# Kernel optimization log

Hardware: AMD Instinct MI355X
Metric: run time of the kernel (lower is better)

## Reference

```python
import jax, jax.numpy as jnp
import numpy as np

H, HK, D, BLK, GH = 32, 8, 96, 64, 128   # q heads, kv heads, head_dim, gate block, gate hidden
HIDDEN = 3072
THR = 0.03
NEG = -1e30

def _rot_half(x):
    h = x.shape[-1] // 2
    return jnp.concatenate([-x[..., h:], x[..., :h]], axis=-1)

def setup_inputs() -> dict:
    key = jax.random.key(0)
    ks = jax.random.split(key, 6)
    B, S = 1, 2048
    hidden_states = jax.random.normal(ks[0], (B, S, HIDDEN), dtype=jnp.float32)
    # RoPE tables, theta = 10000
    inv_freq = 1.0 / (10000.0 ** (np.arange(0, D, 2, dtype=np.float32) / D))
    t = np.arange(S, dtype=np.float32)
    freqs = np.outer(t, inv_freq)                   # [S, D/2]
    emb = np.concatenate([freqs, freqs], axis=-1)   # [S, D]
    cos = jnp.asarray(np.cos(emb), dtype=jnp.float32)
    sin = jnp.asarray(np.sin(emb), dtype=jnp.float32)
    op = H * D + 2 * HK * D
    qkv_w = jax.random.normal(ks[1], (HIDDEN, op), dtype=jnp.float32) * 0.02
    o_w = jax.random.normal(ks[2], (H * D, HIDDEN), dtype=jnp.float32) * 0.02
    gate_wq = jax.random.normal(ks[3], (D, GH), dtype=jnp.float32) * 0.05
    gate_wk = jax.random.normal(ks[4], (2 * D, GH), dtype=jnp.float32) * 0.05
    return dict(hidden_states=hidden_states, cos=cos, sin=sin,
                qkv_w=qkv_w, o_w=o_w, gate_wq=gate_wq, gate_wk=gate_wk)

def reference(hidden_states, cos, sin, qkv_w, o_w, gate_wq, gate_wk):
    B, S, _ = hidden_states.shape
    G = H // HK            # GQA group size
    nB = S // BLK          # number of gate blocks
    scale = D ** -0.5

    # fused QKV projection and head split
    qkv = hidden_states @ qkv_w
    q = qkv[..., : H * D].reshape(B, S, H, D)
    k = qkv[..., H * D : H * D + HK * D].reshape(B, S, HK, D)
    v = qkv[..., H * D + HK * D :].reshape(B, S, HK, D)
    q_nope, k_nope = q, k

    # RoPE (unsqueeze over head dim)
    cs = cos[None, :, None, :]
    sn = sin[None, :, None, :]
    q = q * cs + _rot_half(q) * sn
    k = k * cs + _rot_half(k) * sn

    # ---- learned block-sparse gate (SeerAttention AttnGate) ----
    kb = k_nope.reshape(B, nB, BLK, HK, D)
    k_pool = jnp.concatenate([kb.mean(2), kb.max(2)], axis=-1)      # [B,nB,HK,2D] avg+max seq pooling
    k_gate = jnp.einsum('bnhe,eg->bnhg', k_pool, gate_wk)
    q_pool = q_nope.reshape(B, S, HK, G, D).mean(3)                 # q-head pooling to kv heads
    q_pool = q_pool.reshape(B, nB, BLK, HK, D).mean(2)              # block pooling
    q_gate = jnp.einsum('bnhd,dg->bnhg', q_pool, gate_wq)
    gate_logits = jnp.einsum('bqhg,bkhg->bhqk', q_gate, k_gate) * (GH ** -0.5)
    blk_causal = jnp.tril(jnp.ones((nB, nB), dtype=bool))
    gate_logits = jnp.where(blk_causal, gate_logits, NEG)
    gate_probs = jax.nn.softmax(gate_logits, axis=-1)
    block_mask = (gate_probs >= THR) & blk_causal                   # threshold sparsity method
    block_mask = block_mask | jnp.eye(nB, dtype=bool)               # diagonal block always active

    # expand block mask to token level, intersect with causal mask
    tok_mask = jnp.repeat(jnp.repeat(block_mask, BLK, axis=2), BLK, axis=3)  # [B,HK,S,S]
    causal = jnp.tril(jnp.ones((S, S), dtype=bool))
    mask = tok_mask & causal

    # ---- block-sparse masked attention with GQA ----
    qh = q.transpose(0, 2, 1, 3).reshape(B, HK, G, S, D)
    kh = k.transpose(0, 2, 1, 3)                                    # [B,HK,S,D]
    vh = v.transpose(0, 2, 1, 3)
    scores = jnp.einsum('bhgsd,bhtd->bhgst', qh, kh) * scale
    scores = jnp.where(mask[:, :, None], scores, NEG)
    attn = jax.nn.softmax(scores, axis=-1)
    out = jnp.einsum('bhgst,bhtd->bhgsd', attn, vh)                 # [B,HK,G,S,D]
    out = out.reshape(B, H, S, D).transpose(0, 2, 1, 3).reshape(B, S, H * D)
    return out @ o_w
```

## Files before the change

kernel.cpp:

```cpp
#include <hip/hip_runtime.h>
#include <hip/hip_bf16.h>
#include <math.h>

#define S_LEN 2048
#define HID 3072
#define NHEAD 32
#define NKV 8
#define HDIM 96
#define QKV_N 4608
#define NB 32
#define GHDIM 128
#define KOFF 3072
#define VOFF 3840

typedef __attribute__((ext_vector_type(8))) short bf16x8;
typedef __attribute__((ext_vector_type(4))) short bf16x4;
typedef __attribute__((ext_vector_type(4))) float f32x4;
typedef unsigned short ushort_t;

#define SCALE2 0.14724444754f

__device__ __forceinline__ unsigned short f2bf(float x) {
    unsigned u = __float_as_uint(x);
    u += 0x7fffu + ((u >> 16) & 1u);
    return (unsigned short)(u >> 16);
}
__device__ __forceinline__ unsigned packbf2(float a, float b) {
    return (unsigned)f2bf(a) | ((unsigned)f2bf(b) << 16);
}
__device__ __forceinline__ float bf2f(ushort_t u) {
    return __uint_as_float(((unsigned)u) << 16);
}

#define GLOBAL_AS __attribute__((address_space(1)))
#define LDS_AS __attribute__((address_space(3)))
__device__ __forceinline__ void gl_lds16(const void* g, void* l) {
    __builtin_amdgcn_global_load_lds((const GLOBAL_AS unsigned int*)g,
                                     (LDS_AS unsigned int*)l, 16, 0, 0);
}
__device__ __forceinline__ void barrier_raw() {
    asm volatile("s_barrier" ::: "memory");
}

__global__ __launch_bounds__(256, 4) void gemm_bf16(const ushort_t* __restrict__ A,
                                                    const ushort_t* __restrict__ Bt,
                                                    float* __restrict__ C,
                                                    ushort_t* __restrict__ Cbf,
                                                    float* __restrict__ CfK,
                                                    int M, int N, int K, int mode) {
    __shared__ ushort_t As[128 * 64];
    __shared__ ushort_t Bs[128 * 64];
    const int tid = threadIdx.x;
    const int lane = tid & 63;
    const int w = tid >> 6;
    const int wm = (w >> 1) * 64;
    const int wn = (w & 1) * 64;
    const int l15 = lane & 15;
    const int quad = lane >> 4;
    const int m0 = blockIdx.y * 128;
    const int n0 = blockIdx.x * 128;

    f32x4 acc[4][4] = {};

    for (int k0 = 0; k0 < K; k0 += 64) {
        __syncthreads();
#pragma unroll
        for (int j = 0; j < 4; ++j) {
            int s = j * 256 + w * 64 + lane;
            int row = s >> 3;
            int kc = (s & 7) ^ (row & 7);
            gl_lds16(A + (size_t)(m0 + row) * K + k0 + kc * 8,
                     &As[(j * 256 + w * 64) * 8]);
        }
#pragma unroll
        for (int j = 0; j < 4; ++j) {
            int s = j * 256 + w * 64 + lane;
            int row = s >> 3;
            int kc = (s & 7) ^ (row & 7);
            gl_lds16(Bt + (size_t)(n0 + row) * K + k0 + kc * 8,
                     &Bs[(j * 256 + w * 64) * 8]);
        }
        __syncthreads();
        bf16x8 af[2][4], bf[2][4];
#pragma unroll
        for (int mt = 0; mt < 4; ++mt) {
            int row = wm + mt * 16 + l15;
            int rx = row & 7;
#pragma unroll
            for (int ph = 0; ph < 2; ++ph)
                af[ph][mt] = *(const bf16x8*)&As[(row * 8 + ((ph * 4 + quad) ^ rx)) * 8];
        }
#pragma unroll
        for (int nt = 0; nt < 4; ++nt) {
            int row = wn + nt * 16 + l15;
            int rx = row & 7;
#pragma unroll
            for (int ph = 0; ph < 2; ++ph)
                bf[ph][nt] = *(const bf16x8*)&Bs[(row * 8 + ((ph * 4 + quad) ^ rx)) * 8];
        }
#pragma unroll
        for (int ph = 0; ph < 2; ++ph)
#pragma unroll
            for (int mt = 0; mt < 4; ++mt)
#pragma unroll
                for (int nt = 0; nt < 4; ++nt)
                    acc[mt][nt] = __builtin_amdgcn_mfma_f32_16x16x32_bf16(
                        af[ph][mt], bf[ph][nt], acc[mt][nt], 0, 0, 0);
    }
    if (mode == 0) {
#pragma unroll
        for (int mt = 0; mt < 4; ++mt)
#pragma unroll
            for (int nt = 0; nt < 4; ++nt)
#pragma unroll
                for (int r = 0; r < 4; ++r) {
                    int row = m0 + wm + mt * 16 + quad * 4 + r;
                    int col = n0 + wn + nt * 16 + l15;
                    C[(size_t)row * N + col] = acc[mt][nt][r];
                }
    } else {
        const bool isK = (n0 >= KOFF) && (n0 < VOFF);
#pragma unroll
        for (int mt = 0; mt < 4; ++mt)
#pragma unroll
            for (int nt = 0; nt < 4; ++nt)
#pragma unroll
                for (int r = 0; r < 4; ++r) {
                    int row = m0 + wm + mt * 16 + quad * 4 + r;
                    int col = n0 + wn + nt * 16 + l15;
                    Cbf[(size_t)row * N + col] = f2bf(acc[mt][nt][r]);
                    if (isK) CfK[(size_t)row * 768 + col - KOFF] = acc[mt][nt][r];
                }
    }
}

__device__ __forceinline__ void conv_body(const float* __restrict__ X,
                                          ushort_t* __restrict__ Y, int i) {
    const float4 v = *(const float4*)(X + (size_t)i * 4);
    int2 p;
    p.x = (int)packbf2(v.x, v.y);
    p.y = (int)packbf2(v.z, v.w);
    *(int2*)(Y + (size_t)i * 4) = p;
}

__device__ __forceinline__ void transpose_body(const float* __restrict__ W,
                                               ushort_t* __restrict__ Wt,
                                               int K, int N, int k0, int n0, int tid) {
    __shared__ float Ts[64][65];
    {
        int r = tid >> 2, cq = tid & 3;
#pragma unroll
        for (int i = 0; i < 4; ++i) {
            int c = cq * 16 + i * 4;
            const float4 v = *(const float4*)(W + (size_t)(k0 + r) * N + n0 + c);
            Ts[r][c] = v.x; Ts[r][c + 1] = v.y; Ts[r][c + 2] = v.z; Ts[r][c + 3] = v.w;
        }
    }
    __syncthreads();
#pragma unroll
    for (int it = 0; it < 2; ++it) {
        int n = (tid >> 3) + it * 32;
        int kc = tid & 7;
        int4 r;
        r.x = (int)(packbf2(Ts[kc * 8 + 0][n], Ts[kc * 8 + 1][n]));
        r.y = (int)(packbf2(Ts[kc * 8 + 2][n], Ts[kc * 8 + 3][n]));
        r.z = (int)(packbf2(Ts[kc * 8 + 4][n], Ts[kc * 8 + 5][n]));
        r.w = (int)(packbf2(Ts[kc * 8 + 6][n], Ts[kc * 8 + 7][n]));
        *(int4*)(Wt + (size_t)(n0 + n) * K + k0 + kc * 8) = r;
    }
}

__global__ __launch_bounds__(256) void prep1(const float* __restrict__ hidden,
                                             ushort_t* __restrict__ h_bf,
                                             const float* __restrict__ qkv_w,
                                             ushort_t* __restrict__ w1t) {
    int id = blockIdx.x;
    int tid = threadIdx.x;
    if (id < 6144) {
        conv_body(hidden, h_bf, id * 256 + tid);
    } else {
        int r = id - 6144;
        transpose_body(qkv_w, w1t, HID, QKV_N, (r / 72) * 64, (r % 72) * 64, tid);
    }
}

__global__ __launch_bounds__(256) void prep2(const ushort_t* __restrict__ qkv_bf,
                                             const float* __restrict__ cosb,
                                             const float* __restrict__ sinb,
                                             ushort_t* __restrict__ Qb,
                                             ushort_t* __restrict__ Kb,
                                             ushort_t* __restrict__ Vtb,
                                             const float* __restrict__ o_w,
                                             ushort_t* __restrict__ o_wt) {
    int id = blockIdx.x;
    int tid = threadIdx.x;
    if (id < 15360) {
        int idx = id * 256 + tid;
        int d = idx % 48;
        int tmp = idx / 48;
        int head = tmp % 40;
        int s = tmp / 40;
        float c0 = cosb[s * 96 + d], c1 = cosb[s * 96 + d + 48];
        float s0 = sinb[s * 96 + d], s1 = sinb[s * 96 + d + 48];
        if (head < 32) {
            size_t base = (size_t)s * QKV_N + head * 96;
            float x0 = bf2f(qkv_bf[base + d]), x1 = bf2f(qkv_bf[base + d + 48]);
            size_t ob = (size_t)s * HID + head * 96;
            Qb[ob + d] = f2bf((x0 * c0 - x1 * s0) * SCALE2);
            Qb[ob + d + 48] = f2bf((x1 * c1 + x0 * s1) * SCALE2);
        } else {
            int hh = head - 32;
            size_t base = (size_t)s * QKV_N + KOFF + hh * 96;
            float x0 = bf2f(qkv_bf[base + d]), x1 = bf2f(qkv_bf[base + d + 48]);
            size_t ob = ((size_t)hh * S_LEN + s) * 96;
            Kb[ob + d] = f2bf(x0 * c0 - x1 * s0);
            Kb[ob + d + 48] = f2bf(x1 * c1 + x0 * s1);
        }
    } else if (id < 15616) {
        int r = id - 15360;
        int ibk = r & 31, h = r >> 5;
        __shared__ ushort_t Vs[64][104];
        {
            int rr = tid >> 2, seg = tid & 3;
#pragma unroll
            for (int j = 0; j < 3; ++j) {
                int c = seg * 24 + j * 8;
                const int4 v = *(const int4*)(qkv_bf + (size_t)(ibk * 64 + rr) * QKV_N +
                                              VOFF + h * 96 + c);
                *(int4*)&Vs[rr][c] = v;
            }
        }
        __syncthreads();
#pragma unroll
        for (int it = 0; it < 3; ++it) {
            int s = tid + it * 256;
            int d = s >> 3, tc = s & 7;
            int4 o;
            o.x = (int)Vs[tc * 8 + 0][d] | ((int)Vs[tc * 8 + 1][d] << 16);
            o.y = (int)Vs[tc * 8 + 2][d] | ((int)Vs[tc * 8 + 3][d] << 16);
            o.z = (int)Vs[tc * 8 + 4][d] | ((int)Vs[tc * 8 + 5][d] << 16);
            o.w = (int)Vs[tc * 8 + 6][d] | ((int)Vs[tc * 8 + 7][d] << 16);
            *(int4*)(Vtb + ((size_t)h * 96 + d) * S_LEN + ibk * 64 + tc * 8) = o;
        }
    } else {
        int r = id - 15616;
        transpose_body(o_w, o_wt, HID, HID, (r / 48) * 64, (r % 48) * 64, tid);
    }
}

__global__ __launch_bounds__(256) void pool_gate_kernel(const float* __restrict__ qkvK,
                                                        const ushort_t* __restrict__ qkv_bf,
                                                        const float* __restrict__ gate_wk,
                                                        const float* __restrict__ gate_wq,
                                                        float* __restrict__ k_gate,
                                                        float* __restrict__ q_gate) {
    int nb = blockIdx.x, h = blockIdx.y;
    int tid = threadIdx.x;
    __shared__ float poolk[192];
    __shared__ float poolq[96];
    if (tid < 128) {
        if (tid < 96) {
            float s = 0.f, mx = -1e30f;
            for (int i = 0; i < 64; i++) {
                float v = qkvK[(size_t)(nb * 64 + i) * 768 + h * 96 + tid];
                s += v;
                mx = fmaxf(mx, v);
            }
            poolk[tid] = s * (1.f / 64.f);
            poolk[96 + tid] = mx;
        }
    } else {
        int t2 = tid - 128;
        if (t2 < 96) {
            float s = 0.f;
            for (int i = 0; i < 64; i++)
#pragma unroll
                for (int g = 0; g < 4; g++)
                    s += bf2f(qkv_bf[(size_t)(nb * 64 + i) * QKV_N + (h * 4 + g) * 96 + t2]);
            poolq[t2] = s * (1.f / 256.f);
        }
    }
    __syncthreads();
    if (tid < 128) {
        float acc = 0.f;
        for (int e = 0; e < 192; e++) acc += poolk[e] * gate_wk[e * GHDIM + tid];
        k_gate[(size_t)(nb * NKV + h) * GHDIM + tid] = acc;
    } else {
        int t2 = tid - 128;
        float acc = 0.f;
        for (int e = 0; e < 96; e++) acc += poolq[e] * gate_wq[e * GHDIM + t2];
        q_gate[(size_t)(nb * NKV + h) * GHDIM + t2] = acc;
    }
}

__global__ __launch_bounds__(64) void blockmask_kernel(const float* __restrict__ q_gate,
                                                       const float* __restrict__ k_gate,
                                                       int* __restrict__ mask) {
    int h = blockIdx.x, qb = blockIdx.y;
    int tid = threadIdx.x;
    __shared__ float logits[32];
    if (tid < 32) {
        if (tid <= qb) {
            float acc = 0.f;
            const float* qg = &q_gate[(size_t)(qb * NKV + h) * GHDIM];
            const float* kg = &k_gate[(size_t)(tid * NKV + h) * GHDIM];
            for (int e = 0; e < GHDIM; e++) acc += qg[e] * kg[e];
            logits[tid] = acc * 0.08838834764831845f;
        } else {
            logits[tid] = -1e30f;
        }
    }
    __syncthreads();
    if (tid < 32) {
        float mx = -1e30f;
        for (int j = 0; j <= qb; j++) mx = fmaxf(mx, logits[j]);
        float sum = 0.f;
        for (int j = 0; j <= qb; j++) sum += __expf(logits[j] - mx);
        float p = (tid <= qb) ? __expf(logits[tid] - mx) / sum : 0.f;
        int m = ((p >= 0.03f) && (tid <= qb)) || (tid == qb);
        mask[(h * NB + qb) * NB + tid] = m;
    }
}

__global__ __launch_bounds__(256) void attn_mfma(const ushort_t* __restrict__ Qb,
                                                 const ushort_t* __restrict__ Kb,
                                                 const ushort_t* __restrict__ Vtb,
                                                 const int* __restrict__ mask,
                                                 ushort_t* __restrict__ out) {
    const int hq = blockIdx.x;
    const int ib = NB - 1 - (int)blockIdx.y;
    const int h = hq >> 2;
    const int tid = threadIdx.x;
    const int lane = tid & 63;
    const int w = tid >> 6;
    const int l15 = lane & 15;
    const int quad = lane >> 4;

    __shared__ ushort_t KsL[2][64 * 96];
    __shared__ ushort_t VtL[2][96 * 64];

    int pk[3];
    {
        int b0 = quad + (l15 & 7);
#pragma unroll
        for (int ks = 0; ks < 3; ++ks) {
            int p = b0 + ks * 4;
            if (p >= 12) p -= 12;
            if (p >= 12) p -= 12;
            pk[ks] = p;
        }
    }

    bf16x8 qf[3];
    {
        const ushort_t* qp = Qb + (size_t)(ib * 64 + w * 16 + l15) * HID + hq * 96;
#pragma unroll
        for (int ks = 0; ks < 3; ++ks)
            qf[ks] = *(const bf16x8*)(qp + ks * 32 + quad * 8);
    }

    const ushort_t* kbase = Kb + (size_t)h * S_LEN * 96;
    const ushort_t* vbase = Vtb + (size_t)h * 96 * S_LEN;

    unsigned long long bits =
        __ballot((lane <= ib) && (mask[(h * NB + ib) * NB + (lane & 31)] != 0));

    float m_i = -1e30f, l_i = 0.f;
    f32x4 acc_o[6] = {};

    auto stage = [&](int jb, int buf) {
#pragma unroll
        for (int j = 0; j < 3; ++j) {
            int s = j * 256 + w * 64 + lane;
            int t = (s * 2731) >> 15;
            int cpos = s - t * 12;
            int c = cpos - (t & 7);
            if (c < 0) c += 12;
            gl_lds16(kbase + (size_t)(jb * 64 + t) * 96 + c * 8,
                     &KsL[buf][(j * 256 + w * 64) * 8]);
        }
#pragma unroll
        for (int j = 0; j < 3; ++j) {
            int s = j * 256 + w * 64 + lane;
            int d = s >> 3;
            int tc = (s & 7) ^ (d & 7);
            gl_lds16(vbase + (size_t)d * S_LEN + jb * 64 + tc * 8,
                     &VtL[buf][(j * 256 + w * 64) * 8]);
        }
    };

    int jb = (int)__builtin_ctzll(bits);
    bits &= bits - 1;
    stage(jb, 0);
    int cur = 0;

    while (true) {
        int jn = -1;
        if (bits) {
            jn = (int)__builtin_ctzll(bits);
            bits &= bits - 1;
        }
        if (jn >= 0) {
            stage(jn, cur ^ 1);
            asm volatile("s_waitcnt vmcnt(6)" ::: "memory");
        } else {
            asm volatile("s_waitcnt vmcnt(0)" ::: "memory");
        }
        barrier_raw();

        const ushort_t* Kc = KsL[cur];
        const ushort_t* Vc = VtL[cur];

        f32x4 st[4] = {};
#pragma unroll
        for (int ks = 0; ks < 3; ++ks)
#pragma unroll
            for (int nt = 0; nt < 4; ++nt) {
                bf16x8 kb = *(const bf16x8*)&Kc[(nt * 16 + l15) * 96 + pk[ks] * 8];
                st[nt] = __builtin_amdgcn_mfma_f32_16x16x32_bf16(kb, qf[ks], st[nt], 0, 0, 0);
            }
        if (jb == ib) {
            int q = w * 16 + l15;
#pragma unroll
            for (int nt = 0; nt < 4; ++nt)
#pragma unroll
                for (int r = 0; r < 4; ++r)
                    if ((nt * 16 + quad * 4 + r) > q) st[nt][r] = -1e30f;
        }
        float mx = -1e30f;
#pragma unroll
        for (int nt = 0; nt < 4; ++nt)
#pragma unroll
            for (int r = 0; r < 4; ++r) mx = fmaxf(mx, st[nt][r]);
        mx = fmaxf(mx, __shfl_xor(mx, 16));
        mx = fmaxf(mx, __shfl_xor(mx, 32));
        float mnew = fmaxf(m_i, mx);
        float alpha = __builtin_amdgcn_exp2f(m_i - mnew);
        float ps = 0.f;
#pragma unroll
        for (int nt = 0; nt < 4; ++nt)
#pragma unroll
            for (int r = 0; r < 4; ++r) {
                float p = __builtin_amdgcn_exp2f(st[nt][r] - mnew);
                st[nt][r] = p;
                ps += p;
            }
        ps += __shfl_xor(ps, 16);
        ps += __shfl_xor(ps, 32);
        l_i = l_i * alpha + ps;
        m_i = mnew;
#pragma unroll
        for (int t = 0; t < 6; ++t)
#pragma unroll
            for (int r = 0; r < 4; ++r) acc_o[t][r] *= alpha;
        bf16x4 pf[4];
#pragma unroll
        for (int kblk = 0; kblk < 4; ++kblk) {
            union { bf16x4 v; unsigned u[2]; } pb;
            pb.u[0] = packbf2(st[kblk][0], st[kblk][1]);
            pb.u[1] = packbf2(st[kblk][2], st[kblk][3]);
            pf[kblk] = pb.v;
        }
#pragma unroll
        for (int kblk = 0; kblk < 4; ++kblk) {
            int cchunk = kblk * 2 + (quad >> 1);
            int eoff = (quad & 1) * 4;
#pragma unroll
            for (int dt = 0; dt < 6; ++dt) {
                int d = dt * 16 + l15;
                bf16x4 vf = *(const bf16x4*)&Vc[(d * 8 + (cchunk ^ (d & 7))) * 8 + eoff];
                acc_o[dt] = __builtin_amdgcn_mfma_f32_16x16x16bf16_1k(
                    vf, pf[kblk], acc_o[dt], 0, 0, 0);
            }
        }

        if (jn < 0) break;
        asm volatile("s_waitcnt lgkmcnt(0)" ::: "memory");
        barrier_raw();
        jb = jn;
        cur ^= 1;
    }

    float inv = 1.f / l_i;
    size_t orow = (size_t)(ib * 64 + w * 16 + l15) * HID + hq * 96;
#pragma unroll
    for (int dt = 0; dt < 6; ++dt) {
        int2 pkd;
        pkd.x = (int)packbf2(acc_o[dt][0] * inv, acc_o[dt][1] * inv);
        pkd.y = (int)packbf2(acc_o[dt][2] * inv, acc_o[dt][3] * inv);
        *(int2*)(out + orow + dt * 16 + quad * 4) = pkd;
    }
}

extern "C" void kernel_launch(void* const* d_in, const int* in_sizes, int n_in,
                              void* d_out, int out_size, void* d_ws, size_t ws_size,
                              hipStream_t stream) {
    const float* hidden  = (const float*)d_in[0];
    const float* cosb    = (const float*)d_in[1];
    const float* sinb    = (const float*)d_in[2];
    const float* qkv_w   = (const float*)d_in[3];
    const float* o_w     = (const float*)d_in[4];
    const float* gate_wq = (const float*)d_in[5];
    const float* gate_wk = (const float*)d_in[6];
    float* out = (float*)d_out;

    char* ws = (char*)d_ws;
    ushort_t* qkv_bf   = (ushort_t*)ws;
    float*    qkv_f32K = (float*)(ws + 18874368);
    ushort_t* h_bf     = (ushort_t*)(ws + 25165824);
    ushort_t* w1t      = (ushort_t*)(ws + 37748736);
    ushort_t* attn_out = (ushort_t*)(ws + 66060288);
    ushort_t* Kb       = (ushort_t*)(ws + 78643200);
    ushort_t* Vtb      = (ushort_t*)(ws + 81788928);
    float*    k_gate   = (float*)(ws + 84934656);
    float*    q_gate   = (float*)(ws + 85065728);
    int*      mask     = (int*)(ws + 85196800);
    ushort_t* Qb   = h_bf;
    ushort_t* o_wt = w1t;

    prep1<<<9600, 256, 0, stream>>>(hidden, h_bf, qkv_w, w1t);
    gemm_bf16<<<dim3(QKV_N / 128, S_LEN / 128), 256, 0, stream>>>(
        h_bf, w1t, nullptr, qkv_bf, qkv_f32K, S_LEN, QKV_N, HID, 1);
    pool_gate_kernel<<<dim3(NB, NKV), 256, 0, stream>>>(qkv_f32K, qkv_bf,
                                                        gate_wk, gate_wq, k_gate, q_gate);
    blockmask_kernel<<<dim3(NKV, NB), 64, 0, stream>>>(q_gate, k_gate, mask);
    prep2<<<17920, 256, 0, stream>>>(qkv_bf, cosb, sinb, Qb, Kb, Vtb, o_w, o_wt);
    attn_mfma<<<dim3(NHEAD, NB), 256, 0, stream>>>(Qb, Kb, Vtb, mask, attn_out);
    gemm_bf16<<<dim3(HID / 128, S_LEN / 128), 256, 0, stream>>>(
        attn_out, o_wt, out, nullptr, nullptr, S_LEN, HID, HID, 0);
}
```

Before: 386.7 us.

## Double-buffer GEMM LDS tiles and swizzle workgroup order

Makes the bf16 GEMM double-buffer its A/B tiles in LDS. The next K-slab's global-to-LDS loads are issued before the MFMA work on the current slab, with a partial vmcnt wait, so load latency can overlap compute. It also remaps workgroup IDs in groups of 8 so that consecutive workgroups map to different tiles, which is meant to improve L2 or XCD locality. LDS use doubles to 64KB per block, which may cut occupancy below the launch_bounds target of 4. The swizzle also assumes the workgroup count divides by 8.

```diff
diff --git a/kernel.cpp b/kernel.cpp
--- a/kernel.cpp
+++ b/kernel.cpp
@@ -48,8 +48,8 @@
                                                     ushort_t* __restrict__ Cbf,
                                                     float* __restrict__ CfK,
                                                     int M, int N, int K, int mode) {
-    __shared__ ushort_t As[128 * 64];
-    __shared__ ushort_t Bs[128 * 64];
+    __shared__ ushort_t As[2][128 * 64];
+    __shared__ ushort_t Bs[2][128 * 64];
     const int tid = threadIdx.x;
     const int lane = tid & 63;
     const int w = tid >> 6;
@@ -57,20 +57,25 @@
     const int wn = (w & 1) * 64;
     const int l15 = lane & 15;
     const int quad = lane >> 4;
-    const int m0 = blockIdx.y * 128;
-    const int n0 = blockIdx.x * 128;
+
+    const int nbx = (int)gridDim.x;
+    const int nwg = nbx * (int)gridDim.y;
+    const int bid = (int)blockIdx.y * nbx + (int)blockIdx.x;
+    const int cpx = nwg >> 3;
+    const int swz = (bid & 7) * cpx + (bid >> 3);
+    const int m0 = (swz / nbx) * 128;
+    const int n0 = (swz % nbx) * 128;
 
     f32x4 acc[4][4] = {};
 
-    for (int k0 = 0; k0 < K; k0 += 64) {
-        __syncthreads();
+    auto stage = [&](int k0, int buf) {
 #pragma unroll
         for (int j = 0; j < 4; ++j) {
             int s = j * 256 + w * 64 + lane;
             int row = s >> 3;
             int kc = (s & 7) ^ (row & 7);
             gl_lds16(A + (size_t)(m0 + row) * K + k0 + kc * 8,
-                     &As[(j * 256 + w * 64) * 8]);
+                     &As[buf][(j * 256 + w * 64) * 8]);
         }
 #pragma unroll
         for (int j = 0; j < 4; ++j) {
@@ -78,9 +83,24 @@
             int row = s >> 3;
             int kc = (s & 7) ^ (row & 7);
             gl_lds16(Bt + (size_t)(n0 + row) * K + k0 + kc * 8,
-                     &Bs[(j * 256 + w * 64) * 8]);
-        }
-        __syncthreads();
+                     &Bs[buf][(j * 256 + w * 64) * 8]);
+        }
+    };
+
+    stage(0, 0);
+    int cur = 0;
+
+    for (int k0 = 0; k0 < K; k0 += 64) {
+        if (k0 + 64 < K) {
+            stage(k0 + 64, cur ^ 1);
+            asm volatile("s_waitcnt vmcnt(8)" ::: "memory");
+        } else {
+            asm volatile("s_waitcnt vmcnt(0)" ::: "memory");
+        }
+        barrier_raw();
+
+        const ushort_t* Asc = As[cur];
+        const ushort_t* Bsc = Bs[cur];
         bf16x8 af[2][4], bf[2][4];
 #pragma unroll
         for (int mt = 0; mt < 4; ++mt) {
@@ -88,7 +108,7 @@
             int rx = row & 7;
 #pragma unroll
             for (int ph = 0; ph < 2; ++ph)
-                af[ph][mt] = *(const bf16x8*)&As[(row * 8 + ((ph * 4 + quad) ^ rx)) * 8];
+                af[ph][mt] = *(const bf16x8*)&Asc[(row * 8 + ((ph * 4 + quad) ^ rx)) * 8];
         }
 #pragma unroll
         for (int nt = 0; nt < 4; ++nt) {
@@ -96,7 +116,7 @@
             int rx = row & 7;
 #pragma unroll
             for (int ph = 0; ph < 2; ++ph)
-                bf[ph][nt] = *(const bf16x8*)&Bs[(row * 8 + ((ph * 4 + quad) ^ rx)) * 8];
+                bf[ph][nt] = *(const bf16x8*)&Bsc[(row * 8 + ((ph * 4 + quad) ^ rx)) * 8];
         }
 #pragma unroll
         for (int ph = 0; ph < 2; ++ph)
@@ -106,7 +126,11 @@
                 for (int nt = 0; nt < 4; ++nt)
                     acc[mt][nt] = __builtin_amdgcn_mfma_f32_16x16x32_bf16(
                         af[ph][mt], bf[ph][nt], acc[mt][nt], 0, 0, 0);
-    }
+
+        barrier_raw();
+        cur ^= 1;
+    }
+
     if (mode == 0) {
 #pragma unroll
         for (int mt = 0; mt < 4; ++mt)
```

Measured after the change: 416.7 us. +7.8%, slower.

## Double-buffer A tiles in LDS and load B fragments directly to registers

Applied to the files above, without the earlier changes.

The GEMM main loop now double-buffers the A tile in LDS, prefetching the next k-slice while computing the current one, with explicit vmcnt waits and raw barriers. The B operand no longer goes through LDS. Each wave loads its B fragments straight from global memory into registers, also double-buffered. This is meant to overlap global loads with MFMA work and to remove one LDS round trip. In exchange it uses more registers (occupancy hint lowered from 4 to 2), issues uncoalesced B global reads, and the hand-tuned vmcnt counts must match the exact number of outstanding loads.

```diff
diff --git a/kernel.cpp b/kernel.cpp
--- a/kernel.cpp
+++ b/kernel.cpp
@@ -42,14 +42,13 @@
     asm volatile("s_barrier" ::: "memory");
 }
 
-__global__ __launch_bounds__(256, 4) void gemm_bf16(const ushort_t* __restrict__ A,
+__global__ __launch_bounds__(256, 2) void gemm_bf16(const ushort_t* __restrict__ A,
                                                     const ushort_t* __restrict__ Bt,
                                                     float* __restrict__ C,
                                                     ushort_t* __restrict__ Cbf,
                                                     float* __restrict__ CfK,
                                                     int M, int N, int K, int mode) {
-    __shared__ ushort_t As[128 * 64];
-    __shared__ ushort_t Bs[128 * 64];
+    __shared__ ushort_t As[2][128 * 64];
     const int tid = threadIdx.x;
     const int lane = tid & 63;
     const int w = tid >> 6;
@@ -62,41 +61,37 @@
 
     f32x4 acc[4][4] = {};
 
-    for (int k0 = 0; k0 < K; k0 += 64) {
-        __syncthreads();
+    const ushort_t* BtBase = Bt + (size_t)(n0 + wn + l15) * K + quad * 8;
+
+    auto stageA = [&](int k0, int buf) {
 #pragma unroll
         for (int j = 0; j < 4; ++j) {
             int s = j * 256 + w * 64 + lane;
             int row = s >> 3;
             int kc = (s & 7) ^ (row & 7);
             gl_lds16(A + (size_t)(m0 + row) * K + k0 + kc * 8,
-                     &As[(j * 256 + w * 64) * 8]);
-        }
-#pragma unroll
-        for (int j = 0; j < 4; ++j) {
-            int s = j * 256 + w * 64 + lane;
-            int row = s >> 3;
-            int kc = (s & 7) ^ (row & 7);
-            gl_lds16(Bt + (size_t)(n0 + row) * K + k0 + kc * 8,
-                     &Bs[(j * 256 + w * 64) * 8]);
-        }
-        __syncthreads();
-        bf16x8 af[2][4], bf[2][4];
+                     &As[buf][(j * 256 + w * 64) * 8]);
+        }
+    };
+
+    bf16x8 b0[2][4], b1[2][4];
+    auto loadB = [&](bf16x8 (&bb)[2][4], int k0) {
+#pragma unroll
+        for (int nt = 0; nt < 4; ++nt)
+#pragma unroll
+            for (int ph = 0; ph < 2; ++ph)
+                bb[ph][nt] = *(const bf16x8*)(BtBase + (size_t)nt * 16 * K + k0 + ph * 32);
+    };
+
+    auto compute = [&](int buf, bf16x8 (&bb)[2][4]) {
+        bf16x8 af[2][4];
 #pragma unroll
         for (int mt = 0; mt < 4; ++mt) {
             int row = wm + mt * 16 + l15;
             int rx = row & 7;
 #pragma unroll
             for (int ph = 0; ph < 2; ++ph)
-                af[ph][mt] = *(const bf16x8*)&As[(row * 8 + ((ph * 4 + quad) ^ rx)) * 8];
-        }
-#pragma unroll
-        for (int nt = 0; nt < 4; ++nt) {
-            int row = wn + nt * 16 + l15;
-            int rx = row & 7;
-#pragma unroll
-            for (int ph = 0; ph < 2; ++ph)
-                bf[ph][nt] = *(const bf16x8*)&Bs[(row * 8 + ((ph * 4 + quad) ^ rx)) * 8];
+                af[ph][mt] = *(const bf16x8*)&As[buf][(row * 8 + ((ph * 4 + quad) ^ rx)) * 8];
         }
 #pragma unroll
         for (int ph = 0; ph < 2; ++ph)
@@ -105,8 +100,32 @@
 #pragma unroll
                 for (int nt = 0; nt < 4; ++nt)
                     acc[mt][nt] = __builtin_amdgcn_mfma_f32_16x16x32_bf16(
-                        af[ph][mt], bf[ph][nt], acc[mt][nt], 0, 0, 0);
-    }
+                        af[ph][mt], bb[ph][nt], acc[mt][nt], 0, 0, 0);
+    };
+
+    loadB(b0, 0);
+    stageA(0, 0);
+
+#pragma unroll 1
+    for (int k0 = 0; k0 < K; k0 += 128) {
+        loadB(b1, k0 + 64);
+        stageA(k0 + 64, 1);
+        asm volatile("s_waitcnt vmcnt(12)" ::: "memory");
+        barrier_raw();
+        compute(0, b0);
+        barrier_raw();
+        if (k0 + 128 < K) {
+            loadB(b0, k0 + 128);
+            stageA(k0 + 128, 0);
+            asm volatile("s_waitcnt vmcnt(12)" ::: "memory");
+        } else {
+            asm volatile("s_waitcnt vmcnt(0)" ::: "memory");
+        }
+        barrier_raw();
+        compute(1, b1);
+        barrier_raw();
+    }
+
     if (mode == 0) {
 #pragma unroll
         for (int mt = 0; mt < 4; ++mt)
```

Result: slower. 530.0 us (+37.1%).
